# Kernel optimization log

Measured on AMD Instinct MI355X. Metric: run time of the kernel, lower is better.

Reference implementation:

```python
import jax, jax.numpy as jnp
import numpy as np

DIM = 2048
NUM_HEADS = 16
NUM_KV_HEADS = 4
HEAD_DIM = DIM // NUM_HEADS
B, T = 4, 2048


def setup_inputs() -> dict:
    key = jax.random.key(0)
    ks = jax.random.split(key, 5)
    s_in = 1.0 / np.sqrt(DIM)
    x = jax.random.normal(ks[0], (B, T, DIM), dtype=jnp.float32)
    # weights stored as [in, out] so forward is x @ W (math-equivalent to torch Linear)
    Wq = jax.random.normal(ks[1], (DIM, DIM), dtype=jnp.float32) * s_in
    Wk = jax.random.normal(ks[2], (DIM, NUM_KV_HEADS * HEAD_DIM), dtype=jnp.float32) * s_in
    Wv = jax.random.normal(ks[3], (DIM, NUM_KV_HEADS * HEAD_DIM), dtype=jnp.float32) * s_in
    Wo = jax.random.normal(ks[4], (DIM, DIM), dtype=jnp.float32) * s_in
    return {"x": x, "Wq": Wq, "Wk": Wk, "Wv": Wv, "Wo": Wo}


def _apply_rope(q, k):
    # q: [B, nh, T, hd], k: [B, nkv, T, hd]
    hd = q.shape[-1]
    t = q.shape[2]
    dtype = q.dtype
    freq_seq = jnp.arange(0, hd, 2, dtype=dtype)
    inv_freq = 1.0 / (10000.0 ** (freq_seq / hd))          # [hd/2]
    pos = jnp.arange(t, dtype=dtype)                        # [T]
    sinusoid = pos[:, None] * inv_freq[None, :]             # [T, hd/2]
    sin = jnp.sin(sinusoid)[None, None, :, :]
    cos = jnp.cos(sinusoid)[None, None, :, :]

    def rot(z):
        z1, z2 = z[..., ::2], z[..., 1::2]
        # NOTE: original concatenates (not re-interleaves) the two halves
        return jnp.concatenate([z1 * cos - z2 * sin, z1 * sin + z2 * cos], axis=-1)

    return rot(q), rot(k)


def reference(x, Wq, Wk, Wv, Wo):
    b, t, c = x.shape
    q = (x @ Wq).reshape(b, t, NUM_HEADS, HEAD_DIM).transpose(0, 2, 1, 3)     # [B,nh,T,hd]
    k = (x @ Wk).reshape(b, t, NUM_KV_HEADS, HEAD_DIM).transpose(0, 2, 1, 3)  # [B,nkv,T,hd]
    v = (x @ Wv).reshape(b, t, NUM_KV_HEADS, HEAD_DIM).transpose(0, 2, 1, 3)
    q, k = _apply_rope(q, k)
    # GQA: each KV head serves num_heads // num_kv_heads query heads
    rep = NUM_HEADS // NUM_KV_HEADS
    k = jnp.repeat(k, rep, axis=1)  # [B,nh,T,hd]
    v = jnp.repeat(v, rep, axis=1)
    scale = 1.0 / jnp.sqrt(jnp.asarray(HEAD_DIM, dtype=x.dtype))
    logits = jnp.einsum('bhqd,bhkd->bhqk', q, k) * scale
    causal = jnp.tril(jnp.ones((t, t), dtype=bool))
    logits = jnp.where(causal[None, None, :, :], logits, jnp.finfo(logits.dtype).min)
    attn = jax.nn.softmax(logits, axis=-1)
    out = jnp.einsum('bhqk,bhkd->bhqd', attn, v)            # [B,nh,T,hd]
    out = out.transpose(0, 2, 1, 3).reshape(b, t, c)
    return out @ Wo
```

## Files before the change

### kernel.cpp

```cpp
#include <hip/hip_runtime.h>
#include <stdint.h>
#include <math.h>

#define DEV static __device__ __forceinline__

typedef __attribute__((ext_vector_type(8))) short short8;
typedef __attribute__((ext_vector_type(4))) short short4v;
typedef __attribute__((ext_vector_type(4))) float f32x4;

#define B_ 4
#define T_ 2048
#define H_ 16
#define KVH_ 4
#define HD_ 128
#define DIM_ 2048
#define KVD_ 512
#define BT_ (B_ * T_)
#define KVS_ 1024

DEV float bf2f(unsigned short h) {
  union { uint32_t u; float f; } v; v.u = ((uint32_t)h) << 16; return v.f;
}
DEV unsigned short f2bf(float f) {
  uint32_t u = __builtin_bit_cast(uint32_t, f);
  u += 0x7fffu + ((u >> 16) & 1u);
  return (unsigned short)(u >> 16);
}
DEV void gll16(const void* g, void* l) {
  __builtin_amdgcn_global_load_lds(
      (const __attribute__((address_space(1))) unsigned int*)g,
      (__attribute__((address_space(3))) unsigned int*)l, 16, 0, 0);
}

#if __has_builtin(__builtin_amdgcn_exp2f)
#define EXP2F(x) __builtin_amdgcn_exp2f(x)
#else
#define EXP2F(x) exp2f(x)
#endif

DEV short4v pack4(float a, float b, float c, float d) {
  union { uint32_t u[2]; short4v s; } r;
  asm("v_cvt_pk_bf16_f32 %0, %1, %2" : "=v"(r.u[0]) : "v"(a), "v"(b));
  asm("v_cvt_pk_bf16_f32 %0, %1, %2" : "=v"(r.u[1]) : "v"(c), "v"(d));
  return r.s;
}

#if __has_builtin(__builtin_amdgcn_mfma_f32_16x16x16bf16_1k)
#define MFMA16(A, Bo, C) __builtin_amdgcn_mfma_f32_16x16x16bf16_1k((A), (Bo), (C), 0, 0, 0)
#else
DEV f32x4 mfma16_asm(short4v a, short4v b, f32x4 c) {
  asm volatile("v_mfma_f32_16x16x16_bf16 %0, %1, %2, %0" : "+v"(c) : "v"(a), "v"(b));
  return c;
}
#define MFMA16(A, Bo, C) mfma16_asm((A), (Bo), (C))
#endif

DEV void block_bar() {
  __builtin_amdgcn_sched_barrier(0);
  asm volatile("" ::: "memory");
  __builtin_amdgcn_s_barrier();
  asm volatile("" ::: "memory");
  __builtin_amdgcn_sched_barrier(0);
}

DEV void tr32(const float* __restrict__ W, unsigned short* __restrict__ Wt,
              int R, int C, int bx, int by, int tid) {
  __shared__ float t[32][33];
  int c0 = bx * 32, r0 = by * 32;
  int col = tid & 31;
  int rr = (tid >> 5) * 4;
#pragma unroll
  for (int i = 0; i < 4; ++i)
    t[rr + i][col] = W[(size_t)(r0 + rr + i) * C + c0 + col];
  __syncthreads();
#pragma unroll
  for (int i = 0; i < 4; ++i)
    Wt[(size_t)(c0 + rr + i) * R + r0 + col] = f2bf(t[col][rr + i]);
}

__global__ __launch_bounds__(256) void prep_kernel(
    const float* __restrict__ x, const float* __restrict__ Wq,
    const float* __restrict__ Wk, const float* __restrict__ Wv,
    const float* __restrict__ Wo, unsigned short* __restrict__ xb,
    unsigned short* __restrict__ Wall, unsigned short* __restrict__ Wot) {
  int id = blockIdx.x, tid = threadIdx.x;
  if (id < 8192) {
    size_t idx = (size_t)id * 2048 + tid * 8;
    float4 a = *(const float4*)(x + idx);
    float4 b = *(const float4*)(x + idx + 4);
    short8 o;
    o[0] = (short)f2bf(a.x); o[1] = (short)f2bf(a.y);
    o[2] = (short)f2bf(a.z); o[3] = (short)f2bf(a.w);
    o[4] = (short)f2bf(b.x); o[5] = (short)f2bf(b.y);
    o[6] = (short)f2bf(b.z); o[7] = (short)f2bf(b.w);
    *(short8*)(xb + idx) = o;
  } else if (id < 12288) {
    int t = id - 8192;
    tr32(Wq, Wall, DIM_, DIM_, t & 63, t >> 6, tid);
  } else if (id < 13312) {
    int t = id - 12288;
    tr32(Wk, Wall + (size_t)2048 * DIM_, DIM_, KVD_, t & 15, t >> 4, tid);
  } else if (id < 14336) {
    int t = id - 13312;
    tr32(Wv, Wall + (size_t)2560 * DIM_, DIM_, KVD_, t & 15, t >> 4, tid);
  } else {
    int t = id - 14336;
    tr32(Wo, Wot, DIM_, DIM_, t & 63, t >> 6, tid);
  }
}

__global__ __launch_bounds__(256) void rope_kernel(unsigned short* q,
                                                   unsigned short* kv) {
  int wid = blockIdx.x * 4 + (threadIdx.x >> 6);
  int lane = threadIdx.x & 63;
  const int NQ = B_ * T_ * H_;
  unsigned short* ptr;
  int t;
  if (wid < NQ) {
    int bt = wid >> 4, h = wid & (H_ - 1);
    ptr = q + (size_t)bt * DIM_ + h * HD_;
    t = bt & (T_ - 1);
  } else {
    int id = wid - NQ;
    int bt = id >> 2, g = id & (KVH_ - 1);
    ptr = kv + (size_t)bt * KVS_ + g * HD_;
    t = bt & (T_ - 1);
  }
  float inv = __expf(-(float)lane * 0.14391157f);
  float ang = (float)t * inv;
  float s = sinf(ang), c = cosf(ang);
  uint32_t zz = *(const uint32_t*)(ptr + lane * 2);
  float z1 = bf2f((unsigned short)(zz & 0xffff));
  float z2 = bf2f((unsigned short)(zz >> 16));
  unsigned short o1 = f2bf(z1 * c - z2 * s);
  unsigned short o2 = f2bf(z1 * s + z2 * c);
  ptr[lane] = o1;
  ptr[64 + lane] = o2;
}

__global__ __launch_bounds__(256) void gemm_bt(
    const unsigned short* __restrict__ A, const unsigned short* __restrict__ Bt,
    unsigned short* __restrict__ Cout, int M, int N, int K) {
  __shared__ unsigned short As[128 * 32];
  __shared__ unsigned short Bs[128 * 32];
  int m0 = blockIdx.y * 128, n0 = blockIdx.x * 128;
  int tid = threadIdx.x, w = tid >> 6, l = tid & 63;
  int wr = w >> 1, wc = w & 1;
  int l15 = l & 15, l4 = l >> 4;
  f32x4 acc[4][4] = {};
  for (int k0 = 0; k0 < K; k0 += 32) {
    __syncthreads();
#pragma unroll
    for (int i = 0; i < 2; ++i) {
      int u = i * 256 + w * 64 + l;
      int row = u >> 2, kc = u & 3;
      gll16(A + (size_t)(m0 + row) * K + k0 + kc * 8, As + (size_t)u * 8);
      gll16(Bt + (size_t)(n0 + row) * K + k0 + kc * 8, Bs + (size_t)u * 8);
    }
    __syncthreads();
    short8 a[4], b[4];
#pragma unroll
    for (int mb = 0; mb < 4; ++mb)
      a[mb] = *(const short8*)(As + ((wr * 64 + mb * 16 + l15) * 4 + l4) * 8);
#pragma unroll
    for (int nb = 0; nb < 4; ++nb)
      b[nb] = *(const short8*)(Bs + ((wc * 64 + nb * 16 + l15) * 4 + l4) * 8);
#pragma unroll
    for (int mb = 0; mb < 4; ++mb)
#pragma unroll
      for (int nb = 0; nb < 4; ++nb)
        acc[mb][nb] =
            __builtin_amdgcn_mfma_f32_16x16x32_bf16(a[mb], b[nb], acc[mb][nb], 0, 0, 0);
  }
#pragma unroll
  for (int mb = 0; mb < 4; ++mb)
#pragma unroll
    for (int nb = 0; nb < 4; ++nb)
#pragma unroll
      for (int r = 0; r < 4; ++r) {
        size_t off = (size_t)(m0 + wr * 64 + mb * 16 + l4 * 4 + r) * N +
                     n0 + wc * 64 + nb * 16 + l15;
        Cout[off] = f2bf(acc[mb][nb][r]);
      }
}

#define GEMM256_BODY(A_, Bt_, K_, NX_)                                        \
  __shared__ unsigned short As[4][256 * 32];                                  \
  __shared__ unsigned short Bs[4][256 * 32];                                  \
  int tid = threadIdx.x, w = tid >> 6, l = tid & 63;                          \
  int wm = w >> 2, wn = w & 3;                                                \
  int l15 = l & 15, l4 = l >> 4;                                              \
  int cpx = (int)gridDim.x >> 3;                                              \
  int id = ((int)blockIdx.x & 7) * cpx + ((int)blockIdx.x >> 3);              \
  int bx = id % (NX_), by = id / (NX_);                                       \
  int m0 = by * 256, n0 = bx * 256;                                           \
  int nt = (K_) >> 5;                                                         \
  int u0 = tid * 16;                                                          \
  int ba0 = u0 ^ (((u0 >> 7) & 3) << 4);                                      \
  int r0 = ba0 >> 6;                                                          \
  int c0 = (ba0 & 63) >> 1;                                                   \
  f32x4 acc[8][4] = {};                                                       \
  _Pragma("unroll") for (int tt = 0; tt < 3; ++tt) {                          \
    const unsigned short* a0 = (A_) + (size_t)(m0 + r0) * (K_) + tt * 32 + c0;\
    gll16(a0, &As[tt][tid * 8]);                                              \
    gll16(a0 + (size_t)128 * (K_), &As[tt][4096 + tid * 8]);                  \
    const unsigned short* b0 = (Bt_) + (size_t)(n0 + r0) * (K_) + tt * 32 + c0;\
    gll16(b0, &Bs[tt][tid * 8]);                                              \
    gll16(b0 + (size_t)128 * (K_), &Bs[tt][4096 + tid * 8]);                  \
  }                                                                           \
  asm volatile("s_waitcnt vmcnt(8)" ::: "memory");                            \
  block_bar();                                                                \
  _Pragma("unroll 4") for (int t = 0; t < nt; ++t) {                          \
    int buf = t & 3;                                                          \
    int pf = t + 3;                                                           \
    bool dopf = pf < nt;                                                      \
    int pbuf = pf & 3;                                                        \
    if (dopf) {                                                               \
      const unsigned short* a0 = (A_) + (size_t)(m0 + r0) * (K_) + pf * 32 + c0;\
      gll16(a0, &As[pbuf][tid * 8]);                                          \
      gll16(a0 + (size_t)128 * (K_), &As[pbuf][4096 + tid * 8]);              \
    }                                                                         \
    short8 bfr[4], afr[4];                                                    \
    _Pragma("unroll") for (int nf = 0; nf < 4; ++nf) {                        \
      int row = wn * 64 + nf * 16 + l15;                                      \
      bfr[nf] = *(const short8*)(&Bs[buf][row * 32 + ((l4 ^ ((row >> 1) & 3)) << 3)]);\
    }                                                                         \
    _Pragma("unroll") for (int mf = 0; mf < 4; ++mf) {                        \
      int row = wm * 128 + mf * 16 + l15;                                     \
      afr[mf] = *(const short8*)(&As[buf][row * 32 + ((l4 ^ ((row >> 1) & 3)) << 3)]);\
    }                                                                         \
    asm volatile("s_waitcnt lgkmcnt(0)" ::: "memory");                        \
    __builtin_amdgcn_sched_barrier(0);                                        \
    __builtin_amdgcn_s_setprio(1);                                            \
    _Pragma("unroll") for (int mf = 0; mf < 4; ++mf)                          \
      _Pragma("unroll") for (int nf = 0; nf < 4; ++nf)                        \
        acc[mf][nf] = __builtin_amdgcn_mfma_f32_16x16x32_bf16(afr[mf], bfr[nf], acc[mf][nf], 0, 0, 0);\
    __builtin_amdgcn_s_setprio(0);                                            \
    block_bar();                                                              \
    if (dopf) {                                                               \
      const unsigned short* b0 = (Bt_) + (size_t)(n0 + r0) * (K_) + pf * 32 + c0;\
      gll16(b0, &Bs[pbuf][tid * 8]);                                          \
      gll16(b0 + (size_t)128 * (K_), &Bs[pbuf][4096 + tid * 8]);              \
    }                                                                         \
    short8 afr2[4];                                                           \
    _Pragma("unroll") for (int mf = 0; mf < 4; ++mf) {                        \
      int row = wm * 128 + 64 + mf * 16 + l15;                                \
      afr2[mf] = *(const short8*)(&As[buf][row * 32 + ((l4 ^ ((row >> 1) & 3)) << 3)]);\
    }                                                                         \
    asm volatile("s_waitcnt lgkmcnt(0)" ::: "memory");                        \
    __builtin_amdgcn_sched_barrier(0);                                        \
    __builtin_amdgcn_s_setprio(1);                                            \
    _Pragma("unroll") for (int mf = 0; mf < 4; ++mf)                          \
      _Pragma("unroll") for (int nf = 0; nf < 4; ++nf)                        \
        acc[4 + mf][nf] = __builtin_amdgcn_mfma_f32_16x16x32_bf16(afr2[mf], bfr[nf], acc[4 + mf][nf], 0, 0, 0);\
    __builtin_amdgcn_s_setprio(0);                                            \
    asm volatile("s_waitcnt vmcnt(8)" ::: "memory");                          \
    block_bar();                                                              \
  }

__global__ __launch_bounds__(512, 2) void gemm256_q(
    const unsigned short* __restrict__ A, const unsigned short* __restrict__ Bt,
    unsigned short* __restrict__ Cq) {
  GEMM256_BODY(A, Bt, DIM_, 8)
  const float qs = 0.12752940f;
#pragma unroll
  for (int mf = 0; mf < 8; ++mf)
#pragma unroll
    for (int nf = 0; nf < 4; ++nf)
#pragma unroll
      for (int r = 0; r < 4; ++r) {
        size_t off = (size_t)(m0 + wm * 128 + mf * 16 + l4 * 4 + r) * DIM_ +
                     n0 + wn * 64 + nf * 16 + l15;
        Cq[off] = f2bf(acc[mf][nf][r] * qs);
      }
}

__global__ __launch_bounds__(512, 2) void gemm256_out(
    const unsigned short* __restrict__ A, const unsigned short* __restrict__ Bt,
    float* __restrict__ Cout) {
  GEMM256_BODY(A, Bt, DIM_, 8)
#pragma unroll
  for (int mf = 0; mf < 8; ++mf)
#pragma unroll
    for (int nf = 0; nf < 4; ++nf)
#pragma unroll
      for (int r = 0; r < 4; ++r) {
        size_t off = (size_t)(m0 + wm * 128 + mf * 16 + l4 * 4 + r) * DIM_ +
                     n0 + wn * 64 + nf * 16 + l15;
        Cout[off] = acc[mf][nf][r];
      }
}

__global__ __launch_bounds__(256, 2) void attn_kernel(
    const unsigned short* qws, const unsigned short* __restrict__ kvws,
    unsigned short* ows) {
  int bh = blockIdx.x;
  int qt = 15 - (int)blockIdx.y;
  int b = bh >> 4, h = bh & 15, g = h >> 2;
  int tid = threadIdx.x, w = tid >> 6, l = tid & 63;
  int l15 = l & 15, l4 = l >> 4;

  __shared__ unsigned short Ks[64 * 128];
  __shared__ unsigned short Vt[2][128 * 64];

  const unsigned short* kbase = kvws + (size_t)(b * T_) * KVS_ + g * HD_;
  const unsigned short* vbase = kbase + KVD_;

  int q0 = qt * 128;
  int qw0 = q0 + w * 32;
  int qg = qw0 + l15;

  short8 qf[2][4];
#pragma unroll
  for (int qb = 0; qb < 2; ++qb) {
    const unsigned short* qrow =
        qws + (size_t)(b * T_ + qg + qb * 16) * DIM_ + h * HD_ + l4 * 8;
#pragma unroll
    for (int kc = 0; kc < 4; ++kc) qf[qb][kc] = *(const short8*)(qrow + kc * 32);
  }

  unsigned woff[8];
#pragma unroll
  for (int j = 0; j < 8; ++j)
    woff[j] = (unsigned)(j * 128 + (((l >> 3) ^ j) << 4) + ((l & 7) << 1));

  f32x4 o[2][8] = {};
  float m[2], ls[2];
  m[0] = m[1] = -INFINITY;
  ls[0] = ls[1] = 0.f;

#define STAGE_K(kt_)                                                     \
  {                                                                      \
    const unsigned short* kb = kbase + (size_t)(kt_) * 64 * KVS_;        \
    _Pragma("unroll") for (int i = 0; i < 4; ++i) {                      \
      int u = (i * 4 + w) * 64 + l;                                      \
      int row = u >> 4, c = u & 15;                                      \
      int kc = c ^ (row & 15);                                           \
      gll16(kb + (size_t)row * KVS_ + kc * 8, Ks + (size_t)u * 8);       \
    }                                                                    \
  }
#define VLOAD(kt_)                                                       \
  {                                                                      \
    const unsigned short* vrow = vbase + (size_t)((kt_) * 64 + l) * KVS_;\
    _Pragma("unroll") for (int i = 0; i < 4; ++i)                        \
      vg[i] = *(const short8*)(vrow + (w + i * 4) * 8);                  \
  }
#define VWRITE(buf_)                                                     \
  {                                                                      \
    char* vtb0 = (char*)Vt[buf_] + w * 1024;                             \
    _Pragma("unroll") for (int i = 0; i < 4; ++i)                        \
      _Pragma("unroll") for (int j = 0; j < 8; ++j)                      \
        *(unsigned short*)(vtb0 + i * 4096 + woff[j]) =                  \
            (unsigned short)vg[i][j];                                    \
  }

  short8 vg[4];
  STAGE_K(0);
  VLOAD(0);
  VWRITE(0);
  __syncthreads();

  int nkt = 2 * qt + 2;
  for (int kt = 0; kt < nkt; ++kt) {
    int cur = kt & 1;
    bool pre = (kt + 1 < nkt);
    int kv0 = kt * 64;
    bool active = (kv0 <= qw0 + 31);
    if (pre) VLOAD(kt + 1);

    short4v pb[2][4];
    if (active) {
      f32x4 s[2][4];
      __builtin_amdgcn_s_setprio(1);
#pragma unroll
      for (int nb = 0; nb < 4; ++nb) {
        f32x4 a0 = {}, a1 = {};
#pragma unroll
        for (int kc = 0; kc < 4; ++kc) {
          int row = nb * 16 + l15;
          int c8 = (kc * 4 + l4) ^ l15;
          short8 kf = *(const short8*)(Ks + (row * 16 + c8) * 8);
          a0 = __builtin_amdgcn_mfma_f32_16x16x32_bf16(kf, qf[0][kc], a0, 0, 0, 0);
          a1 = __builtin_amdgcn_mfma_f32_16x16x32_bf16(kf, qf[1][kc], a1, 0, 0, 0);
        }
        s[0][nb] = a0;
        s[1][nb] = a1;
      }
      __builtin_amdgcn_s_setprio(0);
      bool diag = (kv0 + 63 > qw0);
      if (diag) {
#pragma unroll
        for (int qb = 0; qb < 2; ++qb) {
          int qq = qg + qb * 16;
#pragma unroll
          for (int nb = 0; nb < 4; ++nb)
#pragma unroll
            for (int r = 0; r < 4; ++r)
              if ((kv0 + nb * 16 + l4 * 4 + r) > qq) s[qb][nb][r] = -1e30f;
        }
      }
#pragma unroll
      for (int qb = 0; qb < 2; ++qb) {
        float t = -INFINITY;
#pragma unroll
        for (int nb = 0; nb < 4; ++nb)
#pragma unroll
          for (int r = 0; r < 4; ++r) t = fmaxf(t, s[qb][nb][r]);
        t = fmaxf(t, __shfl_xor(t, 16));
        t = fmaxf(t, __shfl_xor(t, 32));
        if (t > m[qb] + 11.5f) {
          float al = EXP2F(m[qb] - t);
          m[qb] = t;
          ls[qb] *= al;
#pragma unroll
          for (int db = 0; db < 8; ++db)
#pragma unroll
            for (int r = 0; r < 4; ++r) o[qb][db][r] *= al;
        }
        float sum = 0.f;
#pragma unroll
        for (int nb = 0; nb < 4; ++nb) {
          float p0 = EXP2F(s[qb][nb][0] - m[qb]);
          float p1 = EXP2F(s[qb][nb][1] - m[qb]);
          float p2 = EXP2F(s[qb][nb][2] - m[qb]);
          float p3 = EXP2F(s[qb][nb][3] - m[qb]);
          sum += (p0 + p1) + (p2 + p3);
          pb[qb][nb] = pack4(p0, p1, p2, p3);
        }
        sum += __shfl_xor(sum, 16);
        sum += __shfl_xor(sum, 32);
        ls[qb] += sum;
      }
    }

    __syncthreads();
    if (pre) STAGE_K(kt + 1);

    if (active) {
      __builtin_amdgcn_s_setprio(1);
#pragma unroll
      for (int db = 0; db < 8; ++db) {
        short4v vf[4];
#pragma unroll
        for (int nb = 0; nb < 4; ++nb) {
          int idx = (db * 16 + l15) * 64 +
                    (((nb * 2 + (l4 >> 1)) ^ (l15 & 7)) << 3) + ((l4 & 1) << 2);
          vf[nb] = *(const short4v*)(Vt[cur] + idx);
        }
#pragma unroll
        for (int qb = 0; qb < 2; ++qb)
#pragma unroll
          for (int nb = 0; nb < 4; ++nb)
            o[qb][db] = MFMA16(vf[nb], pb[qb][nb], o[qb][db]);
      }
      __builtin_amdgcn_s_setprio(0);
    }
    if (pre) VWRITE(1 - cur);
    __syncthreads();
  }

#pragma unroll
  for (int qb = 0; qb < 2; ++qb) {
    float invl = 1.f / ls[qb];
    unsigned short* orow = ows + (size_t)(b * T_ + qg + qb * 16) * DIM_ + h * HD_;
#pragma unroll
    for (int db = 0; db < 8; ++db) {
      short4v pk = pack4(o[qb][db][0] * invl, o[qb][db][1] * invl,
                         o[qb][db][2] * invl, o[qb][db][3] * invl);
      *(short4v*)(orow + db * 16 + l4 * 4) = pk;
    }
  }
#undef STAGE_K
#undef VLOAD
#undef VWRITE
}

extern "C" void kernel_launch(void* const* d_in, const int* in_sizes, int n_in,
                              void* d_out, int out_size, void* d_ws, size_t ws_size,
                              hipStream_t stream) {
  (void)in_sizes; (void)n_in; (void)out_size; (void)ws_size;
  const float* x  = (const float*)d_in[0];
  const float* Wq = (const float*)d_in[1];
  const float* Wk = (const float*)d_in[2];
  const float* Wv = (const float*)d_in[3];
  const float* Wo = (const float*)d_in[4];
  float* out = (float*)d_out;
  char* ws = (char*)d_ws;
  unsigned short* q_ws  = (unsigned short*)(ws + 0);
  unsigned short* kv_ws = (unsigned short*)(ws + 33554432);
  unsigned short* Wall  = (unsigned short*)(ws + 50331648);
  unsigned short* Wot   = (unsigned short*)(ws + 62914560);
  unsigned short* xb = (unsigned short*)d_out;

  prep_kernel<<<18432, 256, 0, stream>>>(x, Wq, Wk, Wv, Wo, xb, Wall, Wot);

  gemm256_q<<<8 * (BT_ / 256), 512, 0, stream>>>(xb, Wall, q_ws);
  gemm_bt<<<dim3(KVS_ / 128, BT_ / 128), 256, 0, stream>>>(
      xb, Wall + (size_t)2048 * DIM_, kv_ws, BT_, KVS_, DIM_);

  rope_kernel<<<(B_ * T_ * (H_ + KVH_)) / 4, 256, 0, stream>>>(q_ws, kv_ws);

  attn_kernel<<<dim3(B_ * H_, T_ / 128), 256, 0, stream>>>(q_ws, kv_ws, q_ws);

  gemm256_out<<<8 * (BT_ / 256), 512, 0, stream>>>(q_ws, Wot, out);
}
```

Before: 356.3 us.

## Fuse RoPE into Q and KV GEMM epilogues using a precomputed cos/sin table

Removes the standalone rope kernel, which re-read and re-wrote all of q and k in bf16. Rotation is now applied in the epilogues of the Q and KV projection GEMMs, using a lane shuffle to fetch each pair partner and writing the de-interleaved halves directly. A cos/sin table is built by extra blocks in the prep kernel and stored in spare output memory. The cost is scattered epilogue stores and table loads inside the GEMMs.

```diff
diff --git a/kernel.cpp b/kernel.cpp
--- a/kernel.cpp
+++ b/kernel.cpp
@@ -82,7 +82,8 @@
     const float* __restrict__ x, const float* __restrict__ Wq,
     const float* __restrict__ Wk, const float* __restrict__ Wv,
     const float* __restrict__ Wo, unsigned short* __restrict__ xb,
-    unsigned short* __restrict__ Wall, unsigned short* __restrict__ Wot) {
+    unsigned short* __restrict__ Wall, unsigned short* __restrict__ Wot,
+    float2* __restrict__ rtab) {
   int id = blockIdx.x, tid = threadIdx.x;
   if (id < 8192) {
     size_t idx = (size_t)id * 2048 + tid * 8;
@@ -103,44 +104,22 @@
   } else if (id < 14336) {
     int t = id - 13312;
     tr32(Wv, Wall + (size_t)2560 * DIM_, DIM_, KVD_, t & 15, t >> 4, tid);
-  } else {
+  } else if (id < 18432) {
     int t = id - 14336;
     tr32(Wo, Wot, DIM_, DIM_, t & 63, t >> 6, tid);
-  }
-}
-
-__global__ __launch_bounds__(256) void rope_kernel(unsigned short* q,
-                                                   unsigned short* kv) {
-  int wid = blockIdx.x * 4 + (threadIdx.x >> 6);
-  int lane = threadIdx.x & 63;
-  const int NQ = B_ * T_ * H_;
-  unsigned short* ptr;
-  int t;
-  if (wid < NQ) {
-    int bt = wid >> 4, h = wid & (H_ - 1);
-    ptr = q + (size_t)bt * DIM_ + h * HD_;
-    t = bt & (T_ - 1);
   } else {
-    int id = wid - NQ;
-    int bt = id >> 2, g = id & (KVH_ - 1);
-    ptr = kv + (size_t)bt * KVS_ + g * HD_;
-    t = bt & (T_ - 1);
-  }
-  float inv = __expf(-(float)lane * 0.14391157f);
-  float ang = (float)t * inv;
-  float s = sinf(ang), c = cosf(ang);
-  uint32_t zz = *(const uint32_t*)(ptr + lane * 2);
-  float z1 = bf2f((unsigned short)(zz & 0xffff));
-  float z2 = bf2f((unsigned short)(zz >> 16));
-  unsigned short o1 = f2bf(z1 * c - z2 * s);
-  unsigned short o2 = f2bf(z1 * s + z2 * c);
-  ptr[lane] = o1;
-  ptr[64 + lane] = o2;
+    int t = (id - 18432) * 4 + (tid >> 6);
+    int j = tid & 63;
+    float inv = __expf(-(float)j * 0.14391157f);
+    float ang = (float)t * inv;
+    rtab[t * 64 + j] = make_float2(cosf(ang), sinf(ang));
+  }
 }
 
 __global__ __launch_bounds__(256) void gemm_bt(
     const unsigned short* __restrict__ A, const unsigned short* __restrict__ Bt,
-    unsigned short* __restrict__ Cout, int M, int N, int K) {
+    const float2* __restrict__ rtab, unsigned short* __restrict__ Cout,
+    int M, int N, int K) {
   __shared__ unsigned short As[128 * 32];
   __shared__ unsigned short Bs[128 * 32];
   int m0 = blockIdx.y * 128, n0 = blockIdx.x * 128;
@@ -172,16 +151,30 @@
         acc[mb][nb] =
             __builtin_amdgcn_mfma_f32_16x16x32_bf16(a[mb], b[nb], acc[mb][nb], 0, 0, 0);
   }
+  int odd = l15 & 1;
 #pragma unroll
   for (int mb = 0; mb < 4; ++mb)
 #pragma unroll
-    for (int nb = 0; nb < 4; ++nb)
+    for (int nb = 0; nb < 4; ++nb) {
+      int cbase = n0 + wc * 64 + nb * 16;
+      bool isK = (cbase < KVD_);
 #pragma unroll
       for (int r = 0; r < 4; ++r) {
-        size_t off = (size_t)(m0 + wr * 64 + mb * 16 + l4 * 4 + r) * N +
-                     n0 + wc * 64 + nb * 16 + l15;
-        Cout[off] = f2bf(acc[mb][nb][r]);
-      }
+        int row = m0 + wr * 64 + mb * 16 + l4 * 4 + r;
+        int c = cbase + l15;
+        float v = acc[mb][nb][r];
+        if (isK) {
+          float pr = __shfl_xor(v, 1);
+          int j = (c & 127) >> 1;
+          float2 cs = rtab[(size_t)(row & (T_ - 1)) * 64 + j];
+          float ov = odd ? (pr * cs.y + v * cs.x) : (v * cs.x - pr * cs.y);
+          int oc = (c & ~127) + j + (odd << 6);
+          Cout[(size_t)row * N + oc] = f2bf(ov);
+        } else {
+          Cout[(size_t)row * N + c] = f2bf(v);
+        }
+      }
+    }
 }
 
 #define GEMM256_BODY(A_, Bt_, K_, NX_)                                        \
@@ -260,18 +253,25 @@
 
 __global__ __launch_bounds__(512, 2) void gemm256_q(
     const unsigned short* __restrict__ A, const unsigned short* __restrict__ Bt,
-    unsigned short* __restrict__ Cq) {
+    const float2* __restrict__ rtab, unsigned short* __restrict__ Cq) {
   GEMM256_BODY(A, Bt, DIM_, 8)
   const float qs = 0.12752940f;
+  int odd = l15 & 1;
 #pragma unroll
   for (int mf = 0; mf < 8; ++mf)
 #pragma unroll
     for (int nf = 0; nf < 4; ++nf)
 #pragma unroll
       for (int r = 0; r < 4; ++r) {
-        size_t off = (size_t)(m0 + wm * 128 + mf * 16 + l4 * 4 + r) * DIM_ +
-                     n0 + wn * 64 + nf * 16 + l15;
-        Cq[off] = f2bf(acc[mf][nf][r] * qs);
+        int row = m0 + wm * 128 + mf * 16 + l4 * 4 + r;
+        int c = n0 + wn * 64 + nf * 16 + l15;
+        float v = acc[mf][nf][r];
+        float pr = __shfl_xor(v, 1);
+        int j = (c & 127) >> 1;
+        float2 cs = rtab[(size_t)(row & (T_ - 1)) * 64 + j];
+        float ov = odd ? (pr * cs.y + v * cs.x) : (v * cs.x - pr * cs.y);
+        int oc = (c & ~127) + j + (odd << 6);
+        Cq[(size_t)row * DIM_ + oc] = f2bf(ov * qs);
       }
 }
 
@@ -491,14 +491,13 @@
   unsigned short* Wall  = (unsigned short*)(ws + 50331648);
   unsigned short* Wot   = (unsigned short*)(ws + 62914560);
   unsigned short* xb = (unsigned short*)d_out;
-
-  prep_kernel<<<18432, 256, 0, stream>>>(x, Wq, Wk, Wv, Wo, xb, Wall, Wot);
-
-  gemm256_q<<<8 * (BT_ / 256), 512, 0, stream>>>(xb, Wall, q_ws);
+  float2* rtab = (float2*)((char*)d_out + 33554432);
+
+  prep_kernel<<<18944, 256, 0, stream>>>(x, Wq, Wk, Wv, Wo, xb, Wall, Wot, rtab);
+
+  gemm256_q<<<8 * (BT_ / 256), 512, 0, stream>>>(xb, Wall, rtab, q_ws);
   gemm_bt<<<dim3(KVS_ / 128, BT_ / 128), 256, 0, stream>>>(
-      xb, Wall + (size_t)2048 * DIM_, kv_ws, BT_, KVS_, DIM_);
-
-  rope_kernel<<<(B_ * T_ * (H_ + KVH_)) / 4, 256, 0, stream>>>(q_ws, kv_ws);
+      xb, Wall + (size_t)2048 * DIM_, rtab, kv_ws, BT_, KVS_, DIM_);
 
   attn_kernel<<<dim3(B_ * H_, T_ / 128), 256, 0, stream>>>(q_ws, kv_ws, q_ws);
 
```

After: 368.3 us. 1.03x slower.
